# Kernel tuning notes

Hardware: AMD Instinct MI355X
Metric: run time of the kernel (lower is better)

The kernel has to match this reference:

```python
import jax, jax.numpy as jnp
import numpy as np

ALPHA = 32.0
RANK = 16
SCALE = ALPHA / RANK


def setup_inputs() -> dict:
    key = jax.random.key(0)
    k1, k2, k3, k4, k5 = jax.random.split(key, 5)
    B, S, D_IN, D_OUT, N = 4, 2048, 4096, 4096, 8
    x = jax.random.normal(k1, (B, S, D_IN), dtype=jnp.float32)
    routing_w = jax.random.uniform(k2, (B, N), dtype=jnp.float32)
    W_base = jax.random.normal(k3, (D_OUT, D_IN), dtype=jnp.float32) * 0.02
    lora_down = jax.random.normal(k4, (N, RANK, D_IN), dtype=jnp.float32) * 0.02
    lora_up = jax.random.normal(k5, (N, D_OUT, RANK), dtype=jnp.float32) * 0.02
    return {"x": x, "routing_w": routing_w, "W_base": W_base,
            "lora_down": lora_down, "lora_up": lora_up}


def reference(x, routing_w, W_base, lora_down, lora_up):
    # base linear: [B,S,D_in] @ [D_out,D_in]^T -> [B,S,D_out]
    base_out = jnp.einsum('bsi,oi->bso', x, W_base)
    # per-expert LoRA down-proj: [B,S,D_in] x [N,R,D_in] -> [B,N,S,R]
    down = jnp.einsum('bsi,nri->bnsr', x, lora_down)
    # up-proj + scale: [B,N,S,R] x [N,D_out,R] -> [B,N,S,D_out]
    up = jnp.einsum('bnsr,nor->bnso', down, lora_up) * SCALE
    # routing-weighted sum over experts: [B,N] x [B,N,S,D_out] -> [B,S,D_out]
    adapter_out = jnp.einsum('bn,bnso->bso', routing_w, up)
    return base_out + adapter_out
```

## Files before the change

kernel.cpp:

```cpp
#include <hip/hip_runtime.h>
#include <hip/hip_bf16.h>
#include <stdint.h>

#define TOK    8192
#define DIN    4096
#define DOUT   4096
#define NEXP   8
#define RK     16
#define NRANK  128
#define KE     4224
#define SEQB   2048
#define LSCALE 2.0f
#define KSPLIT 4
#define KSLICE (DIN / KSPLIT)

typedef __attribute__((ext_vector_type(8))) short bf8_t;
typedef __attribute__((ext_vector_type(4))) float f4_t;

__device__ __forceinline__ void async_copy16(const void* g, void* l) {
  __builtin_amdgcn_global_load_lds((const __attribute__((address_space(1))) void*)g,
                                   (__attribute__((address_space(3))) void*)l,
                                   16, 0, 0);
}

__device__ __forceinline__ ushort f2bf(float f) {
  __hip_bfloat16 h = __float2bfloat16(f);
  return *reinterpret_cast<ushort*>(&h);
}

#define R0 (TOK * DIN / 8)
#define R1 (DOUT * DIN / 8)
#define R2 (DOUT * NEXP * 2)
#define R3 (NRANK * DIN / 8)
#define RTOT (R0 + R1 + R2 + R3)

__global__ __launch_bounds__(256)
void cvt_all_kernel(const float* __restrict__ x, const float* __restrict__ wb,
                    const float* __restrict__ lu, const float* __restrict__ ld,
                    ushort* __restrict__ Xe, ushort* __restrict__ Wc,
                    ushort* __restrict__ Ldb) {
  int i = blockIdx.x * 256 + threadIdx.x;
  const float* src;
  ushort* dst;
  if (i < R0) {
    int t = i >> 9;
    int c = (i & 511) * 8;
    src = x + (size_t)t * DIN + c;
    dst = Xe + (size_t)t * KE + c;
  } else if (i < R0 + R1) {
    int j = i - R0;
    int t = j >> 9;
    int c = (j & 511) * 8;
    src = wb + (size_t)t * DIN + c;
    dst = Wc + (size_t)t * KE + c;
  } else if (i < R0 + R1 + R2) {
    int j = i - (R0 + R1);
    int o = j >> 4;
    int rem = j & 15;
    int n = rem >> 1;
    int half = rem & 1;
    src = lu + ((size_t)n * DOUT + o) * RK + half * 8;
    dst = Wc + (size_t)o * KE + DIN + n * RK + half * 8;
  } else {
    int j = i - (R0 + R1 + R2);
    src = ld + (size_t)j * 8;
    dst = Ldb + (size_t)j * 8;
  }
  const float4* s = reinterpret_cast<const float4*>(src);
  float4 a = s[0], b = s[1];
  union { ushort u[8]; uint4 v; } o;
  o.u[0]=f2bf(a.x); o.u[1]=f2bf(a.y); o.u[2]=f2bf(a.z); o.u[3]=f2bf(a.w);
  o.u[4]=f2bf(b.x); o.u[5]=f2bf(b.y); o.u[6]=f2bf(b.z); o.u[7]=f2bf(b.w);
  *reinterpret_cast<uint4*>(dst) = o.v;
}

template<int KLEN, int LDB, int MODE>
__global__ __launch_bounds__(256)
void gemm128(const ushort* __restrict__ A,
             const ushort* __restrict__ Bm,
             float* __restrict__ C) {
  __shared__ __align__(16) ushort As[128 * 32];
  __shared__ __align__(16) ushort Bs[128 * 32];

  const int tid  = threadIdx.x;
  const int wave = tid >> 6;
  const int lane = tid & 63;

  int bm, bn;
  if (MODE == 0) {
    int bid = blockIdx.x;
    int xcd = bid & 7;
    int idx = bid >> 3;
    int nt  = xcd * 4 + (idx & 3);
    int mt  = idx >> 2;
    bm = mt * 128;
    bn = nt * 128;
  } else {
    bm = blockIdx.y * 128;
    bn = blockIdx.x * 128;
  }
  const int wm = wave & 1, wn = wave >> 1;

  f4_t acc[4][4];
#pragma unroll
  for (int i = 0; i < 4; i++)
#pragma unroll
    for (int j = 0; j < 4; j++) acc[i][j] = (f4_t){0.f, 0.f, 0.f, 0.f};

  const int f0 = tid * 8;
  const int r0 = f0 >> 5, c0 = f0 & 31;
  const int f1 = (256 + tid) * 8;
  const int r1 = f1 >> 5, c1 = f1 & 31;
  const int l0 = (wave << 6) * 8;
  const int l1 = (256 + (wave << 6)) * 8;

  const ushort* Ar = As + (wm * 64 + (lane & 15)) * 32 + (lane >> 4) * 8;
  const ushort* Br = Bs + (wn * 64 + (lane & 15)) * 32 + (lane >> 4) * 8;

  const int kbase = (MODE == 1) ? blockIdx.z * KSLICE : 0;
  const int kend  = kbase + KLEN;

  for (int k0 = kbase; k0 < kend; k0 += 32) {
    __syncthreads();
    async_copy16(A  + (size_t)(bm + r0) * KE  + k0 + c0, (void*)(As + l0));
    async_copy16(A  + (size_t)(bm + r1) * KE  + k0 + c1, (void*)(As + l1));
    async_copy16(Bm + (size_t)(bn + r0) * LDB + k0 + c0, (void*)(Bs + l0));
    async_copy16(Bm + (size_t)(bn + r1) * LDB + k0 + c1, (void*)(Bs + l1));
    __syncthreads();
    bf8_t av[4], bv[4];
#pragma unroll
    for (int i = 0; i < 4; i++) av[i] = *(const bf8_t*)(Ar + i * 16 * 32);
#pragma unroll
    for (int j = 0; j < 4; j++) bv[j] = *(const bf8_t*)(Br + j * 16 * 32);
#pragma unroll
    for (int i = 0; i < 4; i++)
#pragma unroll
      for (int j = 0; j < 4; j++)
        acc[i][j] = __builtin_amdgcn_mfma_f32_16x16x32_bf16(av[i], bv[j], acc[i][j], 0, 0, 0);
  }

  if (MODE == 0) {
#pragma unroll
    for (int i = 0; i < 4; i++) {
      int row = bm + wm * 64 + i * 16 + (lane >> 4) * 4;
#pragma unroll
      for (int j = 0; j < 4; j++) {
        int col = bn + wn * 64 + j * 16 + (lane & 15);
#pragma unroll
        for (int rr = 0; rr < 4; rr++)
          C[(size_t)(row + rr) * DOUT + col] = acc[i][j][rr];
      }
    }
  } else {
    float* Dz = C + (size_t)blockIdx.z * TOK * NRANK;
#pragma unroll
    for (int i = 0; i < 4; i++) {
      int row = bm + wm * 64 + i * 16 + (lane >> 4) * 4;
#pragma unroll
      for (int j = 0; j < 4; j++) {
        int col = wn * 64 + j * 16 + (lane & 15);
#pragma unroll
        for (int rr = 0; rr < 4; rr++)
          Dz[(size_t)(row + rr) * NRANK + col] = acc[i][j][rr];
      }
    }
  }
}

__global__ void scale_store_kernel(const float* __restrict__ D32,
                                   const float* __restrict__ rw,
                                   ushort* __restrict__ Xe) {
  int i = blockIdx.x * 256 + threadIdx.x;
  int t = i >> 5;
  int g = (i & 31) * 4;
  size_t base = (size_t)t * NRANK + g;
  const size_t ss = (size_t)TOK * NRANK;
  float4 a = *reinterpret_cast<const float4*>(D32 + base);
  float4 b = *reinterpret_cast<const float4*>(D32 + ss + base);
  float4 c = *reinterpret_cast<const float4*>(D32 + 2 * ss + base);
  float4 d = *reinterpret_cast<const float4*>(D32 + 3 * ss + base);
  int n = g >> 4;
  int bb = t / SEQB;
  float s = rw[bb * NEXP + n] * LSCALE;
  union { ushort u[4]; uint2 v; } o;
  o.u[0] = f2bf((a.x + b.x + c.x + d.x) * s);
  o.u[1] = f2bf((a.y + b.y + c.y + d.y) * s);
  o.u[2] = f2bf((a.z + b.z + c.z + d.z) * s);
  o.u[3] = f2bf((a.w + b.w + c.w + d.w) * s);
  *reinterpret_cast<uint2*>(Xe + (size_t)t * KE + DIN + g) = o.v;
}

extern "C" void kernel_launch(void* const* d_in, const int* in_sizes, int n_in,
                              void* d_out, int out_size, void* d_ws, size_t ws_size,
                              hipStream_t stream) {
  const float* x  = (const float*)d_in[0];
  const float* rw = (const float*)d_in[1];
  const float* wb = (const float*)d_in[2];
  const float* ld = (const float*)d_in[3];
  const float* lu = (const float*)d_in[4];
  float* out = (float*)d_out;

  ushort* Xe  = (ushort*)d_ws;
  ushort* Wc  = Xe + (size_t)TOK * KE;
  ushort* Ldb = Wc + (size_t)DOUT * KE;
  float*  D32 = (float*)(Ldb + (size_t)NRANK * DIN);

  cvt_all_kernel<<<RTOT / 256, 256, 0, stream>>>(x, wb, lu, ld, Xe, Wc, Ldb);

  gemm128<KSLICE, DIN, 1><<<dim3(1, TOK / 128, KSPLIT), 256, 0, stream>>>(Xe, Ldb, D32);
  scale_store_kernel<<<TOK * NRANK / 4 / 256, 256, 0, stream>>>(D32, rw, Xe);
  gemm128<KE, KE, 0><<<dim3((TOK / 128) * (DOUT / 128)), 256, 0, stream>>>(Xe, Wc, out);
}
```

Measured before the change: 674.7 us.

## Replace main GEMM with 256x256 multi-stage pipelined swizzled LDS kernel

The base+adapter GEMM moves to a new 512-thread kernel with 256x256 tiles. It uses a 4-deep async global-to-LDS ring buffer, XOR-swizzled LDS layout to avoid bank conflicts, and split A/B staging interleaved with MFMA phases under raised wave priority. The aim is to hide global load latency and raise MFMA utilisation compared with the single-buffered 128x128 kernel. The larger LDS footprint limits occupancy to one block per CU, and the hand-tuned waitcnt accounting is fragile.

Measured after the change: 584.7 us. -13.4%, faster.

```diff
diff --git a/kernel.cpp b/kernel.cpp
--- a/kernel.cpp
+++ b/kernel.cpp
@@ -190,6 +190,127 @@
   *reinterpret_cast<uint2*>(Xe + (size_t)t * KE + DIN + g) = o.v;
 }
 
+#define BK32  32
+#define NT132 (KE / BK32)
+
+__global__ __launch_bounds__(512, 2)
+void gemm256(const ushort* __restrict__ A, const ushort* __restrict__ Bm,
+             float* __restrict__ C) {
+  __shared__ __align__(16) ushort As[4][256 * 32];
+  __shared__ __align__(16) ushort Bs[4][256 * 32];
+
+  const int tid  = threadIdx.x;
+  const int w    = tid >> 6;
+  const int lane = tid & 63;
+  const int wm   = w >> 2;
+  const int wn   = w & 3;
+
+  const int bid = blockIdx.x;
+  const int swz = (bid & 7) * 64 + (bid >> 3);
+  const int bm  = (swz & 31) * 256;
+  const int bn  = (swz >> 5) * 256;
+
+  f4_t acc[8][4];
+#pragma unroll
+  for (int i = 0; i < 8; ++i)
+#pragma unroll
+    for (int j = 0; j < 4; ++j) acc[i][j] = (f4_t){0.f, 0.f, 0.f, 0.f};
+
+  const int frow = lane & 15;
+  const int cbs  = (((lane >> 4) ^ (frow >> 1)) << 4);
+  const int ar0  = wm * 128;
+  const int br0  = wn * 64;
+
+  const int sxr = (lane >> 3) << 4;
+  const int t0  = (w << 10) + (lane << 4);
+  const int l0b = t0 ^ sxr;
+  const int l1b = (t0 + 8192) ^ sxr;
+  const size_t goff0 = (size_t)(l0b >> 6) * KE + ((l0b & 63) >> 1);
+  const size_t goff1 = (size_t)(l1b >> 6) * KE + ((l1b & 63) >> 1);
+  const int ld0 = (w << 9);
+  const int ld1 = (w << 9) + 4096;
+
+  const ushort* Ap = A  + (size_t)bm * KE;
+  const ushort* Bp = Bm + (size_t)bn * KE;
+
+#define STAGE_A256(kt, buf) do {                                   \
+    const ushort* cp_ = Ap + (size_t)(kt) * BK32;                  \
+    async_copy16(cp_ + goff0, (void*)(As[buf] + ld0));             \
+    async_copy16(cp_ + goff1, (void*)(As[buf] + ld1));             \
+  } while (0)
+#define STAGE_B256(kt, buf) do {                                   \
+    const ushort* cp_ = Bp + (size_t)(kt) * BK32;                  \
+    async_copy16(cp_ + goff0, (void*)(Bs[buf] + ld0));             \
+    async_copy16(cp_ + goff1, (void*)(Bs[buf] + ld1));             \
+  } while (0)
+
+  STAGE_A256(0, 0); STAGE_B256(0, 0);
+  STAGE_A256(1, 1); STAGE_B256(1, 1);
+  STAGE_A256(2, 2); STAGE_B256(2, 2);
+  asm volatile("s_waitcnt vmcnt(8)" ::: "memory");
+  __builtin_amdgcn_s_barrier();
+
+  for (int T = 0; T < NT132; ++T) {
+    const int b  = T & 3;
+    const int sb = (T + 3) & 3;
+    const char* Ab = (const char*)As[b];
+    const char* Bb = (const char*)Bs[b];
+    bf8_t a0[4], a1[4], bv[4];
+
+#pragma unroll
+    for (int f = 0; f < 4; ++f)
+      a0[f] = *(const bf8_t*)(Ab + (((ar0 + f * 16 + frow) << 6) ^ cbs));
+#pragma unroll
+    for (int g = 0; g < 4; ++g)
+      bv[g] = *(const bf8_t*)(Bb + (((br0 + g * 16 + frow) << 6) ^ cbs));
+    if (T + 3 < NT132) STAGE_A256(T + 3, sb);
+    __builtin_amdgcn_s_barrier();
+    asm volatile("s_waitcnt lgkmcnt(0)" ::: "memory");
+    __builtin_amdgcn_sched_barrier(0);
+    __builtin_amdgcn_s_setprio(1);
+#pragma unroll
+    for (int f = 0; f < 4; ++f)
+#pragma unroll
+      for (int g = 0; g < 4; ++g)
+        acc[f][g] = __builtin_amdgcn_mfma_f32_16x16x32_bf16(a0[f], bv[g], acc[f][g], 0, 0, 0);
+    __builtin_amdgcn_s_setprio(0);
+    __builtin_amdgcn_s_barrier();
+
+#pragma unroll
+    for (int f = 0; f < 4; ++f)
+      a1[f] = *(const bf8_t*)(Ab + (((ar0 + 64 + f * 16 + frow) << 6) ^ cbs));
+    if (T + 3 < NT132) STAGE_B256(T + 3, sb);
+    __builtin_amdgcn_s_barrier();
+    asm volatile("s_waitcnt lgkmcnt(0)" ::: "memory");
+    __builtin_amdgcn_sched_barrier(0);
+    __builtin_amdgcn_s_setprio(1);
+#pragma unroll
+    for (int f = 0; f < 4; ++f)
+#pragma unroll
+      for (int g = 0; g < 4; ++g)
+        acc[4 + f][g] = __builtin_amdgcn_mfma_f32_16x16x32_bf16(a1[f], bv[g], acc[4 + f][g], 0, 0, 0);
+    __builtin_amdgcn_s_setprio(0);
+    if (T < NT132 - 3)       asm volatile("s_waitcnt vmcnt(8)" ::: "memory");
+    else if (T == NT132 - 3) asm volatile("s_waitcnt vmcnt(4)" ::: "memory");
+    else if (T == NT132 - 2) asm volatile("s_waitcnt vmcnt(0)" ::: "memory");
+    __builtin_amdgcn_s_barrier();
+  }
+
+#pragma unroll
+  for (int i = 0; i < 8; ++i) {
+    int row = bm + wm * 128 + i * 16 + (lane >> 4) * 4;
+#pragma unroll
+    for (int j = 0; j < 4; ++j) {
+      int col = bn + wn * 64 + j * 16 + (lane & 15);
+#pragma unroll
+      for (int rr = 0; rr < 4; ++rr)
+        C[(size_t)(row + rr) * DOUT + col] = acc[i][j][rr];
+    }
+  }
+#undef STAGE_A256
+#undef STAGE_B256
+}
+
 extern "C" void kernel_launch(void* const* d_in, const int* in_sizes, int n_in,
                               void* d_out, int out_size, void* d_ws, size_t ws_size,
                               hipStream_t stream) {
@@ -209,5 +330,5 @@
 
   gemm128<KSLICE, DIN, 1><<<dim3(1, TOK / 128, KSPLIT), 256, 0, stream>>>(Xe, Ldb, D32);
   scale_store_kernel<<<TOK * NRANK / 4 / 256, 256, 0, stream>>>(D32, rw, Xe);
-  gemm128<KE, KE, 0><<<dim3((TOK / 128) * (DOUT / 128)), 256, 0, stream>>>(Xe, Wc, out);
-}
+  gemm256<<<dim3((TOK / 256) * (DOUT / 256)), 512, 0, stream>>>(Xe, Wc, out);
+}
```
